# Kernel tuning notes

Hardware: AMD Instinct MI355X
Metric: run time of the kernel (lower is better)

## Reference

```python
import jax, jax.numpy as jnp
import numpy as np

NHEAD = 16
D_MODEL = 1024
D_K = D_MODEL // NHEAD


def setup_inputs() -> dict:
    key = jax.random.key(0)
    ks = jax.random.split(key, 12)
    B, S, D = 2, 2048, D_MODEL
    scale = 1.0 / np.sqrt(D)
    inp = {
        "value": jax.random.normal(ks[0], (B, S, D), dtype=jnp.float32),
        "key": jax.random.normal(ks[1], (B, S, D), dtype=jnp.float32),
        "query": jax.random.normal(ks[2], (B, S, D), dtype=jnp.float32),
        "mask": jax.random.randint(ks[3], (B, 1, S, S), 0, 2, dtype=jnp.int32),
        "Wv": jax.random.normal(ks[4], (D, D), dtype=jnp.float32) * scale,
        "bv": jnp.zeros((D,), dtype=jnp.float32),
        "Wk": jax.random.normal(ks[5], (D, D), dtype=jnp.float32) * scale,
        "bk": jnp.zeros((D,), dtype=jnp.float32),
        "Wq": jax.random.normal(ks[6], (D, D), dtype=jnp.float32) * scale,
        "bq": jnp.zeros((D,), dtype=jnp.float32),
        "Wo": jax.random.normal(ks[7], (D, D), dtype=jnp.float32) * scale,
        "bo": jnp.zeros((D,), dtype=jnp.float32),
    }
    return inp


def reference(value, key, query, mask, Wv, bv, Wk, bk, Wq, bq, Wo, bo):
    B, S, D = value.shape
    H, Dk = NHEAD, D_K

    def proj(x, W, b):
        # nn.Linear: x @ W^T + b, then split heads -> [B, H, S, Dk]
        return (x @ W.T + b).reshape(B, S, H, Dk).transpose(0, 2, 1, 3)

    v = proj(value, Wv, bv)
    k = proj(key, Wk, bk)
    q = proj(query, Wq, bq)

    # NOTE: source code swaps K and V when calling attention():
    #   scores = Q @ V^T / sqrt(d_k);  out = softmax(scores) @ K
    scores = jnp.einsum("bhqd,bhkd->bhqk", q, v) / jnp.sqrt(jnp.float32(Dk))
    scores = jnp.where(mask == 0, jnp.float32(-1e9), scores)
    attn = jax.nn.softmax(scores, axis=-1)  # [B, H, S, S]
    attr_value = jnp.einsum("bhqk,bhkd->bhqd", attn, k)

    out = attr_value.transpose(0, 2, 1, 3).reshape(B, S, H * Dk)
    return out @ Wo.T + bo
```

## Files before the change

### kernel.cpp

```cpp
#include <hip/hip_runtime.h>

#define S_LEN 2048
#define DMODEL 1024
#define NHEADS 16
#define DKH 64

typedef __attribute__((ext_vector_type(8))) short bf16x8;
typedef __attribute__((ext_vector_type(4))) short bf16x4;
typedef __attribute__((ext_vector_type(4))) float f32x4;

#if __has_builtin(__builtin_amdgcn_exp2f)
#define EXP2F(x) __builtin_amdgcn_exp2f(x)
#define QSCALE (0.125f * 1.44269504f)
#else
#define EXP2F(x) __expf(x)
#define QSCALE 0.125f
#endif

static __device__ __forceinline__ short f2bf(float f) {
    unsigned b = __float_as_uint(f);
    b = (b + 0x7FFFu + ((b >> 16) & 1u)) >> 16;
    return (short)b;
}

static __device__ __forceinline__ unsigned pktrunc(float lo, float hi) {
#if __has_builtin(__builtin_amdgcn_perm)
    return __builtin_amdgcn_perm(__float_as_uint(hi), __float_as_uint(lo), 0x07060302u);
#else
    return (__float_as_uint(lo) >> 16) | (__float_as_uint(hi) & 0xFFFF0000u);
#endif
}

static __device__ __forceinline__ f32x4 mfma16(bf16x8 a, bf16x8 b, f32x4 c) {
    return __builtin_amdgcn_mfma_f32_16x16x32_bf16(a, b, c, 0, 0, 0);
}

static __device__ __forceinline__ bf16x8 cat44(bf16x4 a, bf16x4 b) {
    bf16x8 r;
    r[0] = a[0]; r[1] = a[1]; r[2] = a[2]; r[3] = a[3];
    r[4] = b[0]; r[5] = b[1]; r[6] = b[2]; r[7] = b[3];
    return r;
}

static __device__ __forceinline__ void glds16(const short* g, short* l) {
    __builtin_amdgcn_global_load_lds(
        (const __attribute__((address_space(1))) void*)g,
        (__attribute__((address_space(3))) void*)l, 16, 0, 0);
}

struct CvtArgs { const float* src[7]; short* dst[7]; };

__global__ __launch_bounds__(256) void prep(CvtArgs a, const int* __restrict__ mask,
                                            unsigned long long* __restrict__ mw) {
    if (blockIdx.x < 8192) {
        const size_t i8 = ((size_t)blockIdx.x * 256 + threadIdx.x) * 8;
        int seg; size_t off;
        if (i8 < ((size_t)12 << 20)) { seg = (int)(i8 >> 22); off = i8 & ((1u << 22) - 1); }
        else { size_t r = i8 - ((size_t)12 << 20); seg = 3 + (int)(r >> 20); off = r & ((1u << 20) - 1); }
        const float* s = a.src[seg] + off;
        float4 x0 = *(const float4*)s, x1 = *(const float4*)(s + 4);
        short o[8];
        o[0] = f2bf(x0.x); o[1] = f2bf(x0.y); o[2] = f2bf(x0.z); o[3] = f2bf(x0.w);
        o[4] = f2bf(x1.x); o[5] = f2bf(x1.y); o[6] = f2bf(x1.z); o[7] = f2bf(x1.w);
        *(uint4*)(a.dst[seg] + off) = *(uint4*)o;
    } else {
        const int wv = ((blockIdx.x - 8192) << 2) + (threadIdx.x >> 6);
        const int lane = threadIdx.x & 63;
        const size_t base = (size_t)wv << 4;
        #pragma unroll 4
        for (int it = 0; it < 16; ++it) {
            const size_t w = base + it;
            const int m = mask[(w << 6) + lane];
            unsigned long long bal = __ballot(m != 0);
            if (lane == 0) mw[w] = bal;
        }
    }
}

struct GemmArgs { const short* X[3]; const short* W[3]; const float* B[3];
                  void* C[3]; float scale[3]; };

template <int MODE>
__global__ __launch_bounds__(256) void gemm_bt(GemmArgs a) {
    __shared__ short Ah[128 * 64];
    __shared__ short Bh[128 * 64];
    const int z = blockIdx.z;
    const short* X = a.X[z];
    const short* W = a.W[z];
    const float* bias = a.B[z];
    const float scl = a.scale[z];

    const int t = threadIdx.x, wid = t >> 6, lane = t & 63;
    const int l15 = lane & 15, lq = lane >> 4;

    const int lid = blockIdx.x + (blockIdx.y << 5);
    const int vm = ((lid & 7) << 2) + ((lid >> 3) & 3);
    const int vn = lid >> 5;

    int m0, n0;
    if (MODE == 0 && z == 2) { m0 = vn << 7; n0 = vm << 7; }
    else                     { m0 = vm << 7; n0 = vn << 7; }
    const int wm = (wid >> 1) << 6, wn = (wid & 1) << 6;

    const int sr = lane >> 3, pc = lane & 7;
    const int scol = (pc ^ sr) << 3;
    const int arow = (wid << 5) + sr;
    const short* ag = X + (size_t)(m0 + arow) * 1024 + scol;
    const short* bg = W + (size_t)(n0 + arow) * 1024 + scol;
    short* lA = Ah + (wid << 5) * 64;
    short* lB = Bh + (wid << 5) * 64;

    const int key = l15 & 7;
    const int fpk0 = ((lq)     ^ key) << 3;
    const int fpk1 = ((lq + 4) ^ key) << 3;

    f32x4 acc[4][4] = {};

    for (int k0 = 0; k0 < 1024; k0 += 64) {
        __syncthreads();
        glds16(ag,             lA);
        glds16(ag +  8 * 1024, lA +  8 * 64);
        glds16(ag + 16 * 1024, lA + 16 * 64);
        glds16(ag + 24 * 1024, lA + 24 * 64);
        glds16(bg,             lB);
        glds16(bg +  8 * 1024, lB +  8 * 64);
        glds16(bg + 16 * 1024, lB + 16 * 64);
        glds16(bg + 24 * 1024, lB + 24 * 64);
        ag += 64; bg += 64;
        __syncthreads();

        #pragma unroll
        for (int kk = 0; kk < 2; ++kk) {
            const int fp = kk ? fpk1 : fpk0;
            bf16x8 af[4], bfr[4];
            #pragma unroll
            for (int i = 0; i < 4; ++i)
                af[i] = *(const bf16x8*)&Ah[(wm + i * 16 + l15) * 64 + fp];
            #pragma unroll
            for (int j = 0; j < 4; ++j)
                bfr[j] = *(const bf16x8*)&Bh[(wn + j * 16 + l15) * 64 + fp];
            #pragma unroll
            for (int i = 0; i < 4; ++i)
                #pragma unroll
                for (int j = 0; j < 4; ++j)
                    acc[i][j] = mfma16(af[i], bfr[j], acc[i][j]);
        }
    }

    if (MODE == 0 && z == 2) {
        #pragma unroll
        for (int i = 0; i < 4; ++i) {
            #pragma unroll
            for (int r = 0; r < 4; ++r) {
                const int o = m0 + wm + i * 16 + (lq << 2) + r;
                const float bo_ = bias[o];
                const int h = o >> 6, d = o & 63;
                #pragma unroll
                for (int j = 0; j < 4; ++j) {
                    const int n = n0 + wn + j * 16 + l15;
                    const int bb = n >> 11, s = n & 2047;
                    ((short*)a.C[2])[(((size_t)((bb * 16 + h) << 6) + d) << 11) + s] =
                        f2bf(acc[i][j][r] + bo_);
                }
            }
        }
        return;
    }

    #pragma unroll
    for (int j = 0; j < 4; ++j) {
        const int n = n0 + wn + j * 16 + l15;
        const float bn = bias[n];
        #pragma unroll
        for (int i = 0; i < 4; ++i) {
            const int mbase = m0 + wm + i * 16 + (lq << 2);
            #pragma unroll
            for (int r = 0; r < 4; ++r) {
                const float val = (acc[i][j][r] + bn) * scl;
                const int m = mbase + r;
                if (MODE == 0) {
                    const int b = m >> 11, s = m & 2047, h = n >> 6, d = n & 63;
                    ((short*)a.C[z])[((((size_t)(b * 16 + h)) << 11) + s) * 64 + d] = f2bf(val);
                } else {
                    ((float*)a.C[z])[((size_t)m << 10) + n] = val;
                }
            }
        }
    }
}

__global__ __launch_bounds__(256) void gemm1_64(const short* __restrict__ X,
                                                const short* __restrict__ W,
                                                const float* __restrict__ bias,
                                                float* __restrict__ C) {
    __shared__ short Ah[128 * 64];
    __shared__ short Bh[64 * 64];

    const int t = threadIdx.x, wid = t >> 6, lane = t & 63;
    const int l15 = lane & 15, lq = lane >> 4;

    const int lid = blockIdx.x + (blockIdx.y << 5);
    const int vm = ((lid & 7) << 2) + ((lid >> 3) & 3);
    const int vn = lid >> 5;
    const int m0 = vm << 7, n0 = vn << 6;
    const int wm = (wid >> 1) << 6, wn = (wid & 1) << 5;

    const int sr = lane >> 3, pc = lane & 7;
    const int scol = (pc ^ sr) << 3;
    const short* ag = X + (size_t)(m0 + (wid << 5) + sr) * 1024 + scol;
    const short* bg = W + (size_t)(n0 + (wid << 4) + sr) * 1024 + scol;
    short* lA = Ah + (wid << 5) * 64;
    short* lB = Bh + (wid << 4) * 64;

    const int key = l15 & 7;
    const int fpk0 = ((lq)     ^ key) << 3;
    const int fpk1 = ((lq + 4) ^ key) << 3;

    f32x4 acc[4][2] = {};

    for (int k0 = 0; k0 < 1024; k0 += 64) {
        __syncthreads();
        glds16(ag,             lA);
        glds16(ag +  8 * 1024, lA +  8 * 64);
        glds16(ag + 16 * 1024, lA + 16 * 64);
        glds16(ag + 24 * 1024, lA + 24 * 64);
        glds16(bg,             lB);
        glds16(bg +  8 * 1024, lB +  8 * 64);
        ag += 64; bg += 64;
        __syncthreads();

        #pragma unroll
        for (int kk = 0; kk < 2; ++kk) {
            const int fp = kk ? fpk1 : fpk0;
            bf16x8 af[4], bfr[2];
            #pragma unroll
            for (int i = 0; i < 4; ++i)
                af[i] = *(const bf16x8*)&Ah[(wm + i * 16 + l15) * 64 + fp];
            #pragma unroll
            for (int j = 0; j < 2; ++j)
                bfr[j] = *(const bf16x8*)&Bh[(wn + j * 16 + l15) * 64 + fp];
            #pragma unroll
            for (int i = 0; i < 4; ++i)
                #pragma unroll
                for (int j = 0; j < 2; ++j)
                    acc[i][j] = mfma16(af[i], bfr[j], acc[i][j]);
        }
    }

    #pragma unroll
    for (int j = 0; j < 2; ++j) {
        const int n = n0 + wn + j * 16 + l15;
        const float bn = bias[n];
        #pragma unroll
        for (int i = 0; i < 4; ++i) {
            const int mbase = m0 + wm + i * 16 + (lq << 2);
            #pragma unroll
            for (int r = 0; r < 4; ++r)
                C[((size_t)(mbase + r) << 10) + n] = acc[i][j][r] + bn;
        }
    }
}

__global__ __launch_bounds__(256, 4) void attn4(
    const short* __restrict__ Qh, const short* __restrict__ Vh,
    const short* __restrict__ Kt, const unsigned long long* __restrict__ MW,
    short* __restrict__ Opart, float* __restrict__ lpart)
{
    __shared__ short Vs[64 * 64];
    __shared__ short Ks[64 * 64];

    const int t = threadIdx.x, wid = t >> 6, lane = t & 63;
    const int l15 = lane & 15, lq = lane >> 4;
    const int bh = blockIdx.y, b = bh >> 4;
    const int z = blockIdx.z;
    const int ib = (blockIdx.x << 7) + (wid << 5);
    const int jbase = z << 10;

    bf16x8 qf[2][2];
    #pragma unroll
    for (int it = 0; it < 2; ++it) {
        const short* qp = Qh + ((size_t)bh * 2048 + ib + it * 16 + l15) * 64 + (lq << 3);
        qf[it][0] = *(const bf16x8*)qp;
        qf[it][1] = *(const bf16x8*)(qp + 32);
    }

    const int sr = lane >> 3, pc = lane & 7;
    const int lc = pc ^ sr;
    const int wr = wid << 4;
    const short* vsrc = Vh + (size_t)bh * 131072 + (size_t)(jbase + wr + sr) * 64 + (lc << 3);
    const short* ksrc = Kt + (size_t)bh * 131072 + (size_t)(wr + sr) * 2048 + jbase + (lc << 3);
    short* vdst = Vs + (wr << 6);
    short* kdst = Ks + (wr << 6);

    const unsigned long long* mwp0 = MW + ((size_t)b * 2048 + ib + l15) * 32 + (z << 4);
    const unsigned long long* mwp1 = mwp0 + (size_t)16 * 32;

    const int x7 = l15 & 7;
    int voff[2], koff[4];
    #pragma unroll
    for (int p = 0; p < 2; ++p) voff[p] = (((p << 2) + lq) ^ x7) << 3;
    #pragma unroll
    for (int jt = 0; jt < 4; ++jt) {
        const int c8 = (jt << 2) + lq;
        koff[jt] = (((c8 >> 1) ^ x7) << 3) + ((c8 & 1) << 2);
    }

    f32x4 O[2][4] = {};
    f32x4 lsum[2] = {};
    bf16x8 ones8;
    #pragma unroll
    for (int e = 0; e < 8; ++e) ones8[e] = (short)0x3F80;

    for (int jc = 0; jc < 16; ++jc) {
        __syncthreads();
        glds16(vsrc, vdst);
        glds16(vsrc + 512, vdst + 512);
        glds16(ksrc, kdst);
        glds16(ksrc + 8 * 2048, kdst + 512);
        vsrc += 4096; ksrc += 64;

        uint2 mword[2];
        mword[0] = *(const uint2*)(mwp0 + jc);
        mword[1] = *(const uint2*)(mwp1 + jc);
        __syncthreads();

        bf16x8 vf[4][2];
        #pragma unroll
        for (int jt = 0; jt < 4; ++jt) {
            const short* vp = &Vs[((jt << 4) + l15) << 6];
            vf[jt][0] = *(const bf16x8*)(vp + voff[0]);
            vf[jt][1] = *(const bf16x8*)(vp + voff[1]);
        }

        bf16x8 pa[2][2];
        #pragma unroll
        for (int it = 0; it < 2; ++it) {
            const unsigned wx = mword[it].x, wy = mword[it].y;
            #pragma unroll
            for (int b2 = 0; b2 < 2; ++b2) {
                uint4 uu4;
                unsigned* uw = (unsigned*)&uu4;
                #pragma unroll
                for (int h = 0; h < 2; ++h) {
                    const int jt = (b2 << 1) + h;
                    f32x4 sc = {};
                    sc = mfma16(vf[jt][0], qf[it][0], sc);
                    sc = mfma16(vf[jt][1], qf[it][1], sc);
                    const unsigned w32 = (jt < 2) ? wx : wy;
                    float p[4];
                    #pragma unroll
                    for (int r = 0; r < 4; ++r) {
                        const unsigned bit = (w32 >> (((jt & 1) << 4) + (lq << 2) + r)) & 1u;
                        const float e = EXP2F(sc[r]);
                        p[r] = bit ? e : 0.f;
                    }
                    uw[(h << 1) + 0] = pktrunc(p[0], p[1]);
                    uw[(h << 1) + 1] = pktrunc(p[2], p[3]);
                }
                pa[it][b2] = __builtin_bit_cast(bf16x8, uu4);
                lsum[it] = mfma16(pa[it][b2], ones8, lsum[it]);
            }
        }

        #pragma unroll
        for (int dt = 0; dt < 4; ++dt) {
            const short* kp = &Ks[((dt << 4) + l15) << 6];
            #pragma unroll
            for (int b2 = 0; b2 < 2; ++b2) {
                const bf16x4 k0 = *(const bf16x4*)(kp + koff[(b2 << 1) + 0]);
                const bf16x4 k1 = *(const bf16x4*)(kp + koff[(b2 << 1) + 1]);
                const bf16x8 kk = cat44(k0, k1);
                O[0][dt] = mfma16(pa[0][b2], kk, O[0][dt]);
                O[1][dt] = mfma16(pa[1][b2], kk, O[1][dt]);
            }
        }
    }

    const size_t zb = (size_t)((z << 5) + bh) * 2048;
    #pragma unroll
    for (int it = 0; it < 2; ++it) {
        const int rb = ib + (it << 4) + (lq << 2);
        if (l15 == 0) {
            #pragma unroll
            for (int r = 0; r < 4; ++r)
                lpart[zb + rb + r] = lsum[it][r];
        }
        #pragma unroll
        for (int dt = 0; dt < 4; ++dt)
            #pragma unroll
            for (int r = 0; r < 4; ++r)
                Opart[(zb + rb + r) * 64 + (dt << 4) + l15] = f2bf(O[it][dt][r]);
    }
}

__global__ __launch_bounds__(256) void combine(const short* __restrict__ Op,
                                               const float* __restrict__ lp,
                                               short* __restrict__ attr) {
    const int idx = blockIdx.x * 256 + threadIdx.x;
    const int d8 = (idx & 7) << 3;
    const int srow = (idx >> 3) & 2047;
    const int bh = idx >> 14, b = bh >> 4, h = bh & 15;
    const size_t r0 = (size_t)bh * 2048 + srow;
    const size_t r1 = r0 + (size_t)32 * 2048;
    uint4 a = *(const uint4*)(Op + r0 * 64 + d8);
    uint4 c = *(const uint4*)(Op + r1 * 64 + d8);
    const float inv = 1.f / (lp[r0] + lp[r1]);
    const unsigned* au = (const unsigned*)&a;
    const unsigned* cu = (const unsigned*)&c;
    short o[8];
    #pragma unroll
    for (int i = 0; i < 4; ++i) {
        const float a0 = __uint_as_float(au[i] << 16);
        const float a1 = __uint_as_float(au[i] & 0xFFFF0000u);
        const float c0 = __uint_as_float(cu[i] << 16);
        const float c1 = __uint_as_float(cu[i] & 0xFFFF0000u);
        o[2 * i + 0] = f2bf((a0 + c0) * inv);
        o[2 * i + 1] = f2bf((a1 + c1) * inv);
    }
    *(uint4*)&attr[((size_t)b * 2048 + srow) * 1024 + (h << 6) + d8] = *(uint4*)o;
}

extern "C" void kernel_launch(void* const* d_in, const int* in_sizes, int n_in,
                              void* d_out, int out_size, void* d_ws, size_t ws_size,
                              hipStream_t stream) {
    const float* value = (const float*)d_in[0];
    const float* key   = (const float*)d_in[1];
    const float* query = (const float*)d_in[2];
    const int*   mask  = (const int*)d_in[3];
    const float* bv = (const float*)d_in[5];
    const float* bk = (const float*)d_in[7];
    const float* bq = (const float*)d_in[9];
    const float* bo = (const float*)d_in[11];
    float* out = (float*)d_out;

    const size_t M1 = (size_t)1 << 20, M4 = (size_t)1 << 22;
    short* ws = (short*)d_ws;
    short* Xq = ws;
    short* Xk = ws + M4;
    short* Xv = ws + 2 * M4;
    short* Wc0 = ws + 3 * M4;
    short* Wc1 = Wc0 + M1;
    short* Wc2 = Wc1 + M1;
    short* Wc3 = Wc2 + M1;
    short* qh = ws + 4 * M4;
    short* kt = ws + 5 * M4;
    short* vh = ws + 6 * M4;
    unsigned long long* maskw = (unsigned long long*)(ws + 7 * M4);
    short* attr = Xq;
    short* Opart = Xk;
    float* lpart = (float*)Wc0;

    CvtArgs cv;
    cv.src[0] = query; cv.dst[0] = Xq;
    cv.src[1] = key;   cv.dst[1] = Xk;
    cv.src[2] = value; cv.dst[2] = Xv;
    cv.src[3] = (const float*)d_in[8];  cv.dst[3] = Wc0;
    cv.src[4] = (const float*)d_in[6];  cv.dst[4] = Wc1;
    cv.src[5] = (const float*)d_in[4];  cv.dst[5] = Wc2;
    cv.src[6] = (const float*)d_in[10]; cv.dst[6] = Wc3;
    prep<<<10240, 256, 0, stream>>>(cv, mask, maskw);

    GemmArgs g1;
    g1.X[0] = Xq;  g1.W[0] = Wc0; g1.B[0] = bq; g1.C[0] = qh; g1.scale[0] = QSCALE;
    g1.X[1] = Xv;  g1.W[1] = Wc2; g1.B[1] = bv; g1.C[1] = vh; g1.scale[1] = 1.f;
    g1.X[2] = Wc1; g1.W[2] = Xk;  g1.B[2] = bk; g1.C[2] = kt; g1.scale[2] = 1.f;
    gemm_bt<0><<<dim3(32, 8, 3), 256, 0, stream>>>(g1);

    attn4<<<dim3(16, 32, 2), 256, 0, stream>>>(qh, vh, kt, maskw, Opart, lpart);

    combine<<<2048, 256, 0, stream>>>(Opart, lpart, attr);

    gemm1_64<<<dim3(32, 16), 256, 0, stream>>>(attr, Wc3, bo, out);
}
```

Baseline: 256.0 us.

## Fuse split-KV combine and normalization into output projection GEMM A-load

Removes the separate combine kernel and has the output projection GEMM read the two partial attention outputs directly. It sums and normalizes them by the inverse softmax denominators, which are precomputed into shared memory, before writing the A tile to LDS. This avoids writing and rereading the intermediate attr tensor and saves a launch. In exchange, partial outputs are reread by every N-block, the A path goes through registers instead of direct LDS loads, and the next head's loads are prefetched to hide latency.

```diff
diff --git a/kernel.cpp b/kernel.cpp
--- a/kernel.cpp
+++ b/kernel.cpp
@@ -189,12 +189,14 @@
     }
 }
 
-__global__ __launch_bounds__(256) void gemm1_64(const short* __restrict__ X,
-                                                const short* __restrict__ W,
-                                                const float* __restrict__ bias,
-                                                float* __restrict__ C) {
+__global__ __launch_bounds__(256) void gemm1f(const short* __restrict__ Op,
+                                              const float* __restrict__ lp,
+                                              const short* __restrict__ W,
+                                              const float* __restrict__ bias,
+                                              float* __restrict__ C) {
     __shared__ short Ah[128 * 64];
     __shared__ short Bh[64 * 64];
+    __shared__ float invl[16][128];
 
     const int t = threadIdx.x, wid = t >> 6, lane = t & 63;
     const int l15 = lane & 15, lq = lane >> 4;
@@ -205,11 +207,23 @@
     const int m0 = vm << 7, n0 = vn << 6;
     const int wm = (wid >> 1) << 6, wn = (wid & 1) << 5;
 
+    const int bb = m0 >> 11;
+    const int srow0 = m0 & 2047;
+
+    #pragma unroll
+    for (int e = 0; e < 8; ++e) {
+        const int idx = (e << 8) + t;
+        const int h = idx >> 7, rr = idx & 127;
+        const size_t lr0 = ((size_t)(bb * 16 + h)) * 2048 + srow0 + rr;
+        invl[h][rr] = 1.f / (lp[lr0] + lp[lr0 + (size_t)32 * 2048]);
+    }
+
     const int sr = lane >> 3, pc = lane & 7;
     const int scol = (pc ^ sr) << 3;
-    const short* ag = X + (size_t)(m0 + (wid << 5) + sr) * 1024 + scol;
+    const int arow = (wid << 5) + sr;
+    const int srow = srow0 + arow;
     const short* bg = W + (size_t)(n0 + (wid << 4) + sr) * 1024 + scol;
-    short* lA = Ah + (wid << 5) * 64;
+    short* lA = Ah + ((wid << 5) + sr) * 64 + (pc << 3);
     short* lB = Bh + (wid << 4) * 64;
 
     const int key = l15 & 7;
@@ -217,17 +231,43 @@
     const int fpk1 = ((lq + 4) ^ key) << 3;
 
     f32x4 acc[4][2] = {};
-
-    for (int k0 = 0; k0 < 1024; k0 += 64) {
-        __syncthreads();
-        glds16(ag,             lA);
-        glds16(ag +  8 * 1024, lA +  8 * 64);
-        glds16(ag + 16 * 1024, lA + 16 * 64);
-        glds16(ag + 24 * 1024, lA + 24 * 64);
-        glds16(bg,             lB);
-        glds16(bg +  8 * 1024, lB +  8 * 64);
-        ag += 64; bg += 64;
-        __syncthreads();
+    uint4 o0[4], o1[4];
+
+    auto issueA = [&](int h) {
+        #pragma unroll
+        for (int rr = 0; rr < 4; ++rr) {
+            const size_t row = (((size_t)(bb * 16 + h)) << 11) + srow + (rr << 3);
+            o0[rr] = *(const uint4*)(Op + (row << 6) + scol);
+            o1[rr] = *(const uint4*)(Op + ((row + ((size_t)32 << 11)) << 6) + scol);
+        }
+    };
+
+    issueA(0);
+
+    for (int h = 0; h < 16; ++h) {
+        __syncthreads();
+        #pragma unroll
+        for (int rr = 0; rr < 4; ++rr) {
+            const float v = invl[h][arow + (rr << 3)];
+            const unsigned* a0 = (const unsigned*)&o0[rr];
+            const unsigned* a1 = (const unsigned*)&o1[rr];
+            short o[8];
+            #pragma unroll
+            for (int i = 0; i < 4; ++i) {
+                const float x0 = __uint_as_float(a0[i] << 16);
+                const float x1 = __uint_as_float(a0[i] & 0xFFFF0000u);
+                const float y0 = __uint_as_float(a1[i] << 16);
+                const float y1 = __uint_as_float(a1[i] & 0xFFFF0000u);
+                o[2 * i + 0] = f2bf((x0 + y0) * v);
+                o[2 * i + 1] = f2bf((x1 + y1) * v);
+            }
+            *(uint4*)(lA + (rr << 3) * 64) = *(uint4*)o;
+        }
+        glds16(bg, lB);
+        glds16(bg + 8 * 1024, lB + 8 * 64);
+        bg += 64;
+        __syncthreads();
+        if (h < 15) issueA(h + 1);
 
         #pragma unroll
         for (int kk = 0; kk < 2; ++kk) {
@@ -393,33 +433,6 @@
     }
 }
 
-__global__ __launch_bounds__(256) void combine(const short* __restrict__ Op,
-                                               const float* __restrict__ lp,
-                                               short* __restrict__ attr) {
-    const int idx = blockIdx.x * 256 + threadIdx.x;
-    const int d8 = (idx & 7) << 3;
-    const int srow = (idx >> 3) & 2047;
-    const int bh = idx >> 14, b = bh >> 4, h = bh & 15;
-    const size_t r0 = (size_t)bh * 2048 + srow;
-    const size_t r1 = r0 + (size_t)32 * 2048;
-    uint4 a = *(const uint4*)(Op + r0 * 64 + d8);
-    uint4 c = *(const uint4*)(Op + r1 * 64 + d8);
-    const float inv = 1.f / (lp[r0] + lp[r1]);
-    const unsigned* au = (const unsigned*)&a;
-    const unsigned* cu = (const unsigned*)&c;
-    short o[8];
-    #pragma unroll
-    for (int i = 0; i < 4; ++i) {
-        const float a0 = __uint_as_float(au[i] << 16);
-        const float a1 = __uint_as_float(au[i] & 0xFFFF0000u);
-        const float c0 = __uint_as_float(cu[i] << 16);
-        const float c1 = __uint_as_float(cu[i] & 0xFFFF0000u);
-        o[2 * i + 0] = f2bf((a0 + c0) * inv);
-        o[2 * i + 1] = f2bf((a1 + c1) * inv);
-    }
-    *(uint4*)&attr[((size_t)b * 2048 + srow) * 1024 + (h << 6) + d8] = *(uint4*)o;
-}
-
 extern "C" void kernel_launch(void* const* d_in, const int* in_sizes, int n_in,
                               void* d_out, int out_size, void* d_ws, size_t ws_size,
                               hipStream_t stream) {
@@ -446,7 +459,6 @@
     short* kt = ws + 5 * M4;
     short* vh = ws + 6 * M4;
     unsigned long long* maskw = (unsigned long long*)(ws + 7 * M4);
-    short* attr = Xq;
     short* Opart = Xk;
     float* lpart = (float*)Wc0;
 
@@ -468,7 +480,5 @@
 
     attn4<<<dim3(16, 32, 2), 256, 0, stream>>>(qh, vh, kt, maskw, Opart, lpart);
 
-    combine<<<2048, 256, 0, stream>>>(Opart, lpart, attr);
-
-    gemm1_64<<<dim3(32, 16), 256, 0, stream>>>(attr, Wc3, bo, out);
-}
+    gemm1f<<<dim3(32, 16), 256, 0, stream>>>(Opart, lpart, Wc3, bo, out);
+}
```

Result: slower. 263.3 us (+2.8%).
